# Kernel tuning notes

Measured on AMD Instinct MI355X. Metric: run time of the kernel, lower is better.

## Reference

```python
import jax, jax.numpy as jnp
import numpy as np

N_EMBD = 1024
N_HEAD = 16
HEAD_DIM = N_EMBD // N_HEAD
B, S = 4, 1024


def setup_inputs() -> dict:
    key = jax.random.key(0)
    k1, k2, k3 = jax.random.split(key, 3)
    scale = 0.02
    return {
        "x": jax.random.normal(k1, (B, S, N_EMBD), dtype=jnp.float32),
        "Wqkv": jax.random.normal(k2, (N_EMBD, 3 * N_EMBD), dtype=jnp.float32) * scale,
        "bqkv": jnp.zeros((3 * N_EMBD,), dtype=jnp.float32),
        "Wproj": jax.random.normal(k3, (N_EMBD, N_EMBD), dtype=jnp.float32) * scale,
        "bproj": jnp.zeros((N_EMBD,), dtype=jnp.float32),
    }


def reference(x, Wqkv, bqkv, Wproj, bproj):
    b, s, e = x.shape
    qkv = x @ Wqkv + bqkv  # (b, s, 3e)
    q, k, v = jnp.split(qkv, 3, axis=-1)
    # (b, h, s, d)
    q = q.reshape(b, s, N_HEAD, HEAD_DIM).transpose(0, 2, 1, 3)
    k = k.reshape(b, s, N_HEAD, HEAD_DIM).transpose(0, 2, 1, 3)
    v = v.reshape(b, s, N_HEAD, HEAD_DIM).transpose(0, 2, 1, 3)
    scores = jnp.einsum("bhqd,bhkd->bhqk", q, k) / jnp.sqrt(
        jnp.asarray(HEAD_DIM, dtype=x.dtype)
    )
    causal = jnp.tril(jnp.ones((s, s), dtype=bool))  # (s, s)
    scores = jnp.where(causal[None, None, :, :], scores, jnp.asarray(-jnp.inf, dtype=scores.dtype))
    attn = jax.nn.softmax(scores, axis=-1)
    out = jnp.einsum("bhqk,bhkd->bhqd", attn, v)
    out = out.transpose(0, 2, 1, 3).reshape(b, s, e)
    return out @ Wproj + bproj
```

## Files before the change

### kernel.cpp

```cpp
#include <hip/hip_runtime.h>

#define S_LEN 1024
#define EMB   1024
#define NH    16
#define HD    64
#define BATCH 4
#define M_TOT 4096
#define QSZ   (BATCH * NH * S_LEN * HD)

typedef __attribute__((ext_vector_type(4))) float  f32x4;
typedef __attribute__((ext_vector_type(8))) __bf16 bf16x8;

__device__ __forceinline__ unsigned short f2bf(float f) {
  union { float f; unsigned u; } a; a.f = f;
  unsigned r = a.u + 0x7fffu + ((a.u >> 16) & 1u);
  return (unsigned short)(r >> 16);
}

__device__ __forceinline__ float fexp2(float x) {
#if __has_builtin(__builtin_amdgcn_exp2f)
  return __builtin_amdgcn_exp2f(x);
#else
  return exp2f(x);
#endif
}

__global__ __launch_bounds__(256) void prep(
    const float* __restrict__ x, const float* __restrict__ Wqkv,
    const float* __restrict__ Wproj,
    unsigned short* __restrict__ xb, unsigned short* __restrict__ WqkvT,
    unsigned short* __restrict__ WprojT)
{
  __shared__ unsigned short tile[32][33];
  const int bid = blockIdx.x;
  if (bid < 4096) {
    const int i = bid * 256 + threadIdx.x;
    float4 v = ((const float4*)x)[i];
    ushort4 o;
    o.x = f2bf(v.x); o.y = f2bf(v.y); o.z = f2bf(v.z); o.w = f2bf(v.w);
    ((ushort4*)xb)[i] = o;
    return;
  }
  const float* in; unsigned short* out; int N, n0, k0;
  if (bid < 7168) {
    const int b2 = bid - 4096;
    in = Wqkv; out = WqkvT; N = 3 * EMB;
    n0 = (b2 % 96) * 32; k0 = (b2 / 96) * 32;
  } else {
    const int b3 = bid - 7168;
    in = Wproj; out = WprojT; N = EMB;
    n0 = (b3 % 32) * 32; k0 = (b3 / 32) * 32;
  }
  const int tx = threadIdx.x & 31, ty = threadIdx.x >> 5;
  #pragma unroll
  for (int r = ty; r < 32; r += 8)
    tile[r][tx] = f2bf(in[(size_t)(k0 + r) * N + n0 + tx]);
  __syncthreads();
  #pragma unroll
  for (int r = ty; r < 32; r += 8)
    out[(size_t)(n0 + r) * EMB + k0 + tx] = tile[tx][r];
}

template<int EPI>
__global__ __launch_bounds__(512, 4) void gemm_tile(
    const unsigned short* __restrict__ A,
    const unsigned short* __restrict__ Bt,
    const float* __restrict__ bias,
    void* __restrict__ outp,
    int K, int Nout)
{
  __shared__ alignas(16) char smem[65536];
  const int m0 = blockIdx.x * 128, n0 = blockIdx.y * 128;
  const int t = threadIdx.x;
  const int wid = t >> 6, lane = t & 63;
  const int wm = wid >> 2, wn = wid & 3;
  const int lr = lane & 15, lg = lane >> 4;
  const int nkt = K >> 6;

  f32x4 acc[4][2] = {};

  auto STAGE = [&](int b, int kt) {
    const int k0 = kt << 6;
    #pragma unroll
    for (int l = 0; l < 2; ++l) {
      const int L = l * 8192 + t * 16;
      const int row = L >> 7, c = (L >> 4) & 7;
      const int ce = (c ^ (row & 7)) << 3;
      const unsigned short* gA = A  + (size_t)(m0 + row) * K + k0 + ce;
      const unsigned short* gB = Bt + (size_t)(n0 + row) * K + k0 + ce;
      __builtin_amdgcn_global_load_lds(
          (const __attribute__((address_space(1))) unsigned int*)gA,
          (__attribute__((address_space(3))) unsigned int*)(smem + b * 32768 + L),
          16, 0, 0);
      __builtin_amdgcn_global_load_lds(
          (const __attribute__((address_space(1))) unsigned int*)gB,
          (__attribute__((address_space(3))) unsigned int*)(smem + b * 32768 + 16384 + L),
          16, 0, 0);
    }
  };

  STAGE(0, 0);

  for (int kt = 0; kt < nkt; ++kt) {
    const int cur = kt & 1;
    if (kt + 1 < nkt) {
      STAGE(cur ^ 1, kt + 1);
      asm volatile("s_waitcnt vmcnt(4)" ::: "memory");
    } else {
      asm volatile("s_waitcnt vmcnt(0)" ::: "memory");
    }
    __builtin_amdgcn_s_barrier();
    asm volatile("" ::: "memory");

    const char* Ab = smem + cur * 32768;
    const char* Bb = Ab + 16384;
    bf16x8 af[4][2], bfr[2][2];
    #pragma unroll
    for (int i = 0; i < 4; ++i)
      #pragma unroll
      for (int kk = 0; kk < 2; ++kk) {
        const int row = wm * 64 + i * 16 + lr;
        af[i][kk] = *(const bf16x8*)(Ab + row * 128 + (((kk * 4 + lg) ^ (row & 7)) << 4));
      }
    #pragma unroll
    for (int j = 0; j < 2; ++j)
      #pragma unroll
      for (int kk = 0; kk < 2; ++kk) {
        const int row = wn * 32 + j * 16 + lr;
        bfr[j][kk] = *(const bf16x8*)(Bb + row * 128 + (((kk * 4 + lg) ^ (row & 7)) << 4));
      }
    __builtin_amdgcn_s_setprio(1);
    #pragma unroll
    for (int i = 0; i < 4; ++i)
      #pragma unroll
      for (int j = 0; j < 2; ++j)
        #pragma unroll
        for (int kk = 0; kk < 2; ++kk)
          acc[i][j] = __builtin_amdgcn_mfma_f32_16x16x32_bf16(af[i][kk], bfr[j][kk], acc[i][j], 0, 0, 0);
    __builtin_amdgcn_s_setprio(0);

    asm volatile("s_waitcnt lgkmcnt(0)" ::: "memory");
    __builtin_amdgcn_s_barrier();
  }

  if (EPI == 0) {
    unsigned short* O = (unsigned short*)outp;
    const int sec = n0 >> 10;
    if (sec < 2) {
      #pragma unroll
      for (int i = 0; i < 4; ++i)
        #pragma unroll
        for (int j = 0; j < 2; ++j) {
          const int col = n0 + wn * 32 + j * 16 + lr;
          const float bv = bias[col];
          const int cc = col & 1023, h = cc >> 6, d = cc & 63;
          #pragma unroll
          for (int r = 0; r < 4; ++r) {
            const int row = m0 + wm * 64 + i * 16 + lg * 4 + r;
            float v = acc[i][j][r] + bv;
            if (sec == 0) v *= 0.18033688f;
            const int bb = row >> 10, ss = row & 1023;
            O[(size_t)sec * QSZ + (((size_t)(bb * NH + h) * S_LEN + ss) * HD + d)] = f2bf(v);
          }
        }
    } else {
      unsigned short* T = (unsigned short*)smem;
      #pragma unroll
      for (int i = 0; i < 4; ++i)
        #pragma unroll
        for (int j = 0; j < 2; ++j) {
          const int ci = wn * 32 + j * 16 + lr;
          const float bv = bias[n0 + ci];
          union { ushort4 s4; __bf16 b[4]; } pk;
          #pragma unroll
          for (int r = 0; r < 4; ++r) pk.b[r] = (__bf16)(acc[i][j][r] + bv);
          *(ushort4*)(T + ci * 136 + wm * 64 + i * 16 + lg * 4) = pk.s4;
        }
      __syncthreads();
      const int ci = t >> 2, part = t & 3;
      const int cc = (n0 - 2048) + ci;
      const int h = cc >> 6, d = cc & 63;
      const int bb2 = m0 >> 10, sbase = m0 & 1023;
      unsigned short* dst = O + 2ull * QSZ +
          ((size_t)(bb2 * NH + h) * HD + d) * S_LEN + sbase;
      #pragma unroll
      for (int u = 0; u < 4; ++u) {
        const int spos = part * 32 + u * 8;
        *(bf16x8*)(dst + spos) = *(const bf16x8*)(T + ci * 136 + spos);
      }
    }
  } else {
    float* Of = (float*)outp;
    #pragma unroll
    for (int i = 0; i < 4; ++i)
      #pragma unroll
      for (int j = 0; j < 2; ++j) {
        const int col = n0 + wn * 32 + j * 16 + lr;
        const float bv = bias[col];
        #pragma unroll
        for (int r = 0; r < 4; ++r) {
          const int row = m0 + wm * 64 + i * 16 + lg * 4 + r;
          Of[(size_t)row * (size_t)Nout + col] = acc[i][j][r] + bv;
        }
      }
  }
}

__device__ __forceinline__ void group_tile(
    const bf16x8 (&kf)[8], const bf16x8 (&vf)[8], const bf16x8 (&qf)[2],
    int kt, int q0, bool diag, int lr, int lg,
    float& m, float& lp, f32x4 (&o)[4])
{
  f32x4 sacc[4] = {};
  __builtin_amdgcn_s_setprio(1);
  #pragma unroll
  for (int nt = 0; nt < 4; ++nt)
    #pragma unroll
    for (int kk = 0; kk < 2; ++kk)
      sacc[nt] = __builtin_amdgcn_mfma_f32_16x16x32_bf16(kf[nt * 2 + kk], qf[kk], sacc[nt], 0, 0, 0);
  __builtin_amdgcn_s_setprio(0);

  float p[16];
  if (diag) {
    const int q = q0 + lr;
    #pragma unroll
    for (int nt = 0; nt < 4; ++nt)
      #pragma unroll
      for (int r = 0; r < 4; ++r) {
        int k = kt * 64 + nt * 16 + lg * 4 + r;
        p[nt * 4 + r] = (k > q) ? -1e30f : sacc[nt][r];
      }
  } else {
    #pragma unroll
    for (int nt = 0; nt < 4; ++nt)
      #pragma unroll
      for (int r = 0; r < 4; ++r)
        p[nt * 4 + r] = sacc[nt][r];
  }

  float r8[8], r4[4];
  #pragma unroll
  for (int i = 0; i < 8; ++i) r8[i] = fmaxf(p[i], p[i + 8]);
  #pragma unroll
  for (int i = 0; i < 4; ++i) r4[i] = fmaxf(r8[i], r8[i + 4]);
  float pm = fmaxf(fmaxf(r4[0], r4[1]), fmaxf(r4[2], r4[3]));
  if (__any(pm > m + 11.5f)) {
    float px = fmaxf(pm, __shfl_xor(pm, 16, 64));
    px = fmaxf(px, __shfl_xor(px, 32, 64));
    float mn = fmaxf(m, px);
    float fs = fexp2(m - mn);
    lp *= fs;
    #pragma unroll
    for (int dt = 0; dt < 4; ++dt)
      #pragma unroll
      for (int r = 0; r < 4; ++r) o[dt][r] *= fs;
    m = mn;
  }
  #pragma unroll
  for (int i = 0; i < 16; ++i) p[i] = fexp2(p[i] - m);

  float s8[8], s4[4];
  #pragma unroll
  for (int i = 0; i < 8; ++i) s8[i] = p[i] + p[i + 8];
  #pragma unroll
  for (int i = 0; i < 4; ++i) s4[i] = s8[i] + s8[i + 4];
  lp += (s4[0] + s4[1]) + (s4[2] + s4[3]);

  union { unsigned u[8]; __bf16 b[16]; } W;
  #pragma unroll
  for (int i = 0; i < 16; ++i) W.b[i] = (__bf16)p[i];

  const int dl0 = ((2 * (lg & 1) + (lg >> 1)) * 16 + lr) << 2;
  const int dl1 = ((2 * ((lg & 1) ^ 1) + (lg >> 1)) * 16 + lr) << 2;
  const bool oddlg = (lg & 1) != 0;
  const bool hb    = (lg >> 1) != 0;
  union { unsigned u[4]; bf16x8 v; } T0, T1;
  #pragma unroll
  for (int kk = 0; kk < 2; ++kk) {
    #pragma unroll
    for (int c = 0; c < 2; ++c) {
      unsigned vlo = W.u[4 * kk + c];
      unsigned vhi = W.u[4 * kk + 2 + c];
      unsigned s0 = oddlg ? vhi : vlo;
      unsigned s1 = oddlg ? vlo : vhi;
      unsigned r0 = (unsigned)__builtin_amdgcn_ds_permute(dl0, (int)s0);
      unsigned r1 = (unsigned)__builtin_amdgcn_ds_permute(dl1, (int)s1);
      unsigned* T = kk ? T1.u : T0.u;
      T[c]     = hb ? r1 : r0;
      T[2 + c] = hb ? r0 : r1;
    }
  }

  __builtin_amdgcn_s_setprio(1);
  #pragma unroll
  for (int dt = 0; dt < 4; ++dt) {
    o[dt] = __builtin_amdgcn_mfma_f32_16x16x32_bf16(vf[dt * 2 + 0], T0.v, o[dt], 0, 0, 0);
    o[dt] = __builtin_amdgcn_mfma_f32_16x16x32_bf16(vf[dt * 2 + 1], T1.v, o[dt], 0, 0, 0);
  }
  __builtin_amdgcn_s_setprio(0);
}

__device__ __forceinline__ void group_epilogue(
    const f32x4 (&o)[4], float lp, int q0, int lr, int lg,
    char* Ep, unsigned short* __restrict__ attout, int bb, int h)
{
  float l2 = lp + __shfl_xor(lp, 16, 64);
  float l4 = l2 + __shfl_xor(l2, 32, 64);
  float rl = 1.0f / l4;
  #pragma unroll
  for (int dt = 0; dt < 4; ++dt) {
    union { ushort4 s4; __bf16 b[4]; } ov;
    #pragma unroll
    for (int r = 0; r < 4; ++r) ov.b[r] = (__bf16)(o[dt][r] * rl);
    int byt = (lr * 128 + (dt * 16 + lg * 4) * 2) ^ ((lr & 7) << 4);
    *(ushort4*)(Ep + byt) = ov.s4;
  }
  asm volatile("s_waitcnt lgkmcnt(0)" ::: "memory");
  const int lane = lr + lg * 16;
  const int ql = lane >> 2, c = lane & 3;
  #pragma unroll
  for (int s = 0; s < 2; ++s) {
    int byt = (ql * 128 + (c * 16 + s * 8) * 2) ^ ((ql & 7) << 4);
    bf16x8 vrow = *(const bf16x8*)(Ep + byt);
    *(bf16x8*)(attout + (size_t)(bb * S_LEN + q0 + ql) * EMB + h * HD + c * 16 + s * 8) = vrow;
  }
}

__global__ __launch_bounds__(256, 2) void attn_fwd(
    const unsigned short* __restrict__ Q,
    const unsigned short* __restrict__ K,
    const unsigned short* __restrict__ Vt,
    unsigned short* __restrict__ attout)
{
  __shared__ alignas(16) char stage[3][16384];
  __shared__ alignas(16) char Ep_lds[4][2048];
  const int bid = blockIdx.x;
  const int bh   = ((bid & 7) << 3) | ((bid >> 3) & 7);
  const int base = bid >> 6;
  const int wv = threadIdx.x >> 6, lane = threadIdx.x & 63;
  const int pi = base * 4 + wv;
  const int lr = lane & 15, lg = lane >> 4;
  const int nkt  = 16 - base;
  const int nktl = base + 1;
  const int q0h = (63 - pi) * 16, q0l = pi * 16;
  const unsigned short* Qb = Q  + (size_t)bh * (S_LEN * HD);
  const unsigned short* Kh = K  + (size_t)bh * (S_LEN * HD);
  const unsigned short* Vh = Vt + (size_t)bh * (HD * S_LEN);
  const int bb = bh >> 4, h = bh & 15;

  auto STAGE = [&](int b, int kt) {
    char* lb = &stage[b][0];
    #pragma unroll
    for (int j = 0; j < 4; ++j) {
      if (wv < 2) {
        int L = wv * 4096 + j * 1024 + lane * 16;
        int row = L >> 7, c = (L >> 4) & 7;
        const unsigned short* src = Kh + (size_t)(kt * 64 + row) * HD + ((c ^ (row & 7)) << 3);
        __builtin_amdgcn_global_load_lds(
            (const __attribute__((address_space(1))) unsigned int*)src,
            (__attribute__((address_space(3))) unsigned int*)(lb + wv * 4096 + j * 1024),
            16, 0, 0);
      } else {
        int L = (wv - 2) * 4096 + j * 1024 + lane * 16;
        int row = L >> 7, c = (L >> 4) & 7;
        const unsigned short* src = Vh + (size_t)row * S_LEN + kt * 64 + ((c ^ (row & 7)) << 3);
        __builtin_amdgcn_global_load_lds(
            (const __attribute__((address_space(1))) unsigned int*)src,
            (__attribute__((address_space(3))) unsigned int*)(lb + 8192 + (wv - 2) * 4096 + j * 1024),
            16, 0, 0);
      }
    }
  };

  bf16x8 qfh[2], qfl[2];
  #pragma unroll
  for (int kk = 0; kk < 2; ++kk) {
    qfh[kk] = *(const bf16x8*)(Qb + (size_t)(q0h + lr) * HD + kk * 32 + lg * 8);
    qfl[kk] = *(const bf16x8*)(Qb + (size_t)(q0l + lr) * HD + kk * 32 + lg * 8);
  }

  float mh = -1e30f, lph = 0.f, ml = -1e30f, lpl = 0.f;
  f32x4 oh[4] = {}, ol[4] = {};

  STAGE(0, 0);
  STAGE(1, 1);

  for (int kt = 0; kt < nkt; ++kt) {
    if (kt + 2 < nkt) {
      STAGE((kt + 2) % 3, kt + 2);
      asm volatile("s_waitcnt vmcnt(8)" ::: "memory");
    } else if (kt + 1 < nkt) {
      asm volatile("s_waitcnt vmcnt(4)" ::: "memory");
    } else {
      asm volatile("s_waitcnt vmcnt(0)" ::: "memory");
    }
    __builtin_amdgcn_s_barrier();
    asm volatile("" ::: "memory");

    const char* sb = &stage[kt % 3][0];
    bf16x8 kf[8], vf[8];
    #pragma unroll
    for (int nt = 0; nt < 4; ++nt)
      #pragma unroll
      for (int kk = 0; kk < 2; ++kk) {
        const int byt = (nt * 16 + lr) * 128 + ((((kk << 2) + lg) ^ (lr & 7)) << 4);
        kf[nt * 2 + kk] = *(const bf16x8*)(sb + byt);
        vf[nt * 2 + kk] = *(const bf16x8*)(sb + 8192 + byt);
      }

    group_tile(kf, vf, qfh, kt, q0h, kt == nkt - 1, lr, lg, mh, lph, oh);
    if (kt < nktl)
      group_tile(kf, vf, qfl, kt, q0l, kt == nktl - 1, lr, lg, ml, lpl, ol);

    asm volatile("s_waitcnt lgkmcnt(0)" ::: "memory");
    __builtin_amdgcn_s_barrier();
  }

  char* Ep = &Ep_lds[wv][0];
  group_epilogue(oh, lph, q0h, lr, lg, Ep, attout, bb, h);
  group_epilogue(ol, lpl, q0l, lr, lg, Ep, attout, bb, h);
}

extern "C" void kernel_launch(void* const* d_in, const int* in_sizes, int n_in,
                              void* d_out, int out_size, void* d_ws, size_t ws_size,
                              hipStream_t stream) {
  const float* x     = (const float*)d_in[0];
  const float* Wqkv  = (const float*)d_in[1];
  const float* bqkv  = (const float*)d_in[2];
  const float* Wproj = (const float*)d_in[3];
  const float* bproj = (const float*)d_in[4];

  unsigned short* xb     = (unsigned short*)d_ws;
  unsigned short* WqkvT  = xb     + (size_t)M_TOT * EMB;
  unsigned short* WprojT = WqkvT  + (size_t)3 * EMB * EMB;
  unsigned short* qkv    = WprojT + (size_t)EMB * EMB;
  unsigned short* att    = qkv    + 3ull * QSZ;

  prep<<<dim3(8192), dim3(256), 0, stream>>>(x, Wqkv, Wproj, xb, WqkvT, WprojT);

  gemm_tile<0><<<dim3(M_TOT / 128, 3 * EMB / 128), dim3(512), 0, stream>>>(
      xb, WqkvT, bqkv, (void*)qkv, EMB, 0);

  attn_fwd<<<dim3(8 * BATCH * NH), dim3(256), 0, stream>>>(
      qkv, qkv + QSZ, qkv + 2ull * QSZ, att);

  gemm_tile<1><<<dim3(M_TOT / 128, EMB / 128), dim3(512), 0, stream>>>(
      att, WprojT, bproj, d_out, EMB, EMB);
}
```

Baseline: 85.65 us.

## Deepen software pipelines in GEMM and attention, drop trailing barriers

The GEMM mainloop moves from a 64-wide K tile with double buffering to a 32-wide K tile with triple buffering. Each prefetch is issued after the current tile's LDS reads, and the end-of-iteration barrier is removed. The attention kernel goes from three to four K/V stages in the same style, prefetching three tiles ahead with one barrier per iteration. This aims to hide more global latency and cut synchronisation, at the cost of more LDS in attention and half as much MFMA work per barrier in the GEMM.

```diff
diff --git a/kernel.cpp b/kernel.cpp
--- a/kernel.cpp
+++ b/kernel.cpp
@@ -69,78 +69,70 @@
     void* __restrict__ outp,
     int K, int Nout)
 {
-  __shared__ alignas(16) char smem[65536];
+  __shared__ alignas(16) char smem[49152];
   const int m0 = blockIdx.x * 128, n0 = blockIdx.y * 128;
   const int t = threadIdx.x;
   const int wid = t >> 6, lane = t & 63;
   const int wm = wid >> 2, wn = wid & 3;
   const int lr = lane & 15, lg = lane >> 4;
-  const int nkt = K >> 6;
+  const int nkt = K >> 5;
 
   f32x4 acc[4][2] = {};
 
   auto STAGE = [&](int b, int kt) {
-    const int k0 = kt << 6;
-    #pragma unroll
-    for (int l = 0; l < 2; ++l) {
-      const int L = l * 8192 + t * 16;
-      const int row = L >> 7, c = (L >> 4) & 7;
-      const int ce = (c ^ (row & 7)) << 3;
-      const unsigned short* gA = A  + (size_t)(m0 + row) * K + k0 + ce;
-      const unsigned short* gB = Bt + (size_t)(n0 + row) * K + k0 + ce;
-      __builtin_amdgcn_global_load_lds(
-          (const __attribute__((address_space(1))) unsigned int*)gA,
-          (__attribute__((address_space(3))) unsigned int*)(smem + b * 32768 + L),
-          16, 0, 0);
-      __builtin_amdgcn_global_load_lds(
-          (const __attribute__((address_space(1))) unsigned int*)gB,
-          (__attribute__((address_space(3))) unsigned int*)(smem + b * 32768 + 16384 + L),
-          16, 0, 0);
-    }
+    const int k0 = kt << 5;
+    const int L = t * 16;
+    const int row = L >> 6;
+    const int c = (L >> 4) & 3;
+    const int ce = (c ^ (row & 3)) << 3;
+    const unsigned short* gA = A  + (size_t)(m0 + row) * K + k0 + ce;
+    const unsigned short* gB = Bt + (size_t)(n0 + row) * K + k0 + ce;
+    __builtin_amdgcn_global_load_lds(
+        (const __attribute__((address_space(1))) unsigned int*)gA,
+        (__attribute__((address_space(3))) unsigned int*)(smem + b * 16384 + L),
+        16, 0, 0);
+    __builtin_amdgcn_global_load_lds(
+        (const __attribute__((address_space(1))) unsigned int*)gB,
+        (__attribute__((address_space(3))) unsigned int*)(smem + b * 16384 + 8192 + L),
+        16, 0, 0);
   };
 
   STAGE(0, 0);
+  STAGE(1, 1);
 
   for (int kt = 0; kt < nkt; ++kt) {
-    const int cur = kt & 1;
     if (kt + 1 < nkt) {
-      STAGE(cur ^ 1, kt + 1);
-      asm volatile("s_waitcnt vmcnt(4)" ::: "memory");
+      asm volatile("s_waitcnt vmcnt(2)" ::: "memory");
     } else {
       asm volatile("s_waitcnt vmcnt(0)" ::: "memory");
     }
     __builtin_amdgcn_s_barrier();
     asm volatile("" ::: "memory");
 
-    const char* Ab = smem + cur * 32768;
-    const char* Bb = Ab + 16384;
-    bf16x8 af[4][2], bfr[2][2];
+    const char* Ab = smem + (kt % 3) * 16384;
+    const char* Bb = Ab + 8192;
+    bf16x8 af[4], bfr[2];
+    #pragma unroll
+    for (int i = 0; i < 4; ++i) {
+      const int row = wm * 64 + i * 16 + lr;
+      af[i] = *(const bf16x8*)(Ab + row * 64 + ((lg ^ (row & 3)) << 4));
+    }
+    #pragma unroll
+    for (int j = 0; j < 2; ++j) {
+      const int row = wn * 32 + j * 16 + lr;
+      bfr[j] = *(const bf16x8*)(Bb + row * 64 + ((lg ^ (row & 3)) << 4));
+    }
+    if (kt + 2 < nkt) STAGE((kt + 2) % 3, kt + 2);
+
+    __builtin_amdgcn_s_setprio(1);
     #pragma unroll
     for (int i = 0; i < 4; ++i)
       #pragma unroll
-      for (int kk = 0; kk < 2; ++kk) {
-        const int row = wm * 64 + i * 16 + lr;
-        af[i][kk] = *(const bf16x8*)(Ab + row * 128 + (((kk * 4 + lg) ^ (row & 7)) << 4));
-      }
-    #pragma unroll
-    for (int j = 0; j < 2; ++j)
-      #pragma unroll
-      for (int kk = 0; kk < 2; ++kk) {
-        const int row = wn * 32 + j * 16 + lr;
-        bfr[j][kk] = *(const bf16x8*)(Bb + row * 128 + (((kk * 4 + lg) ^ (row & 7)) << 4));
-      }
-    __builtin_amdgcn_s_setprio(1);
-    #pragma unroll
-    for (int i = 0; i < 4; ++i)
-      #pragma unroll
       for (int j = 0; j < 2; ++j)
-        #pragma unroll
-        for (int kk = 0; kk < 2; ++kk)
-          acc[i][j] = __builtin_amdgcn_mfma_f32_16x16x32_bf16(af[i][kk], bfr[j][kk], acc[i][j], 0, 0, 0);
+        acc[i][j] = __builtin_amdgcn_mfma_f32_16x16x32_bf16(af[i], bfr[j], acc[i][j], 0, 0, 0);
     __builtin_amdgcn_s_setprio(0);
 
     asm volatile("s_waitcnt lgkmcnt(0)" ::: "memory");
-    __builtin_amdgcn_s_barrier();
   }
 
   if (EPI == 0) {
@@ -165,6 +157,7 @@
         }
     } else {
       unsigned short* T = (unsigned short*)smem;
+      __syncthreads();
       #pragma unroll
       for (int i = 0; i < 4; ++i)
         #pragma unroll
@@ -332,7 +325,7 @@
     const unsigned short* __restrict__ Vt,
     unsigned short* __restrict__ attout)
 {
-  __shared__ alignas(16) char stage[3][16384];
+  __shared__ alignas(16) char stage[4][16384];
   __shared__ alignas(16) char Ep_lds[4][2048];
   const int bid = blockIdx.x;
   const int bh   = ((bid & 7) << 3) | ((bid >> 3) & 7);
@@ -384,10 +377,10 @@
 
   STAGE(0, 0);
   STAGE(1, 1);
+  STAGE(2, 2);
 
   for (int kt = 0; kt < nkt; ++kt) {
     if (kt + 2 < nkt) {
-      STAGE((kt + 2) % 3, kt + 2);
       asm volatile("s_waitcnt vmcnt(8)" ::: "memory");
     } else if (kt + 1 < nkt) {
       asm volatile("s_waitcnt vmcnt(4)" ::: "memory");
@@ -397,7 +390,7 @@
     __builtin_amdgcn_s_barrier();
     asm volatile("" ::: "memory");
 
-    const char* sb = &stage[kt % 3][0];
+    const char* sb = &stage[kt & 3][0];
     bf16x8 kf[8], vf[8];
     #pragma unroll
     for (int nt = 0; nt < 4; ++nt)
@@ -407,13 +400,13 @@
         kf[nt * 2 + kk] = *(const bf16x8*)(sb + byt);
         vf[nt * 2 + kk] = *(const bf16x8*)(sb + 8192 + byt);
       }
+    if (kt + 3 < nkt) STAGE((kt + 3) & 3, kt + 3);
 
     group_tile(kf, vf, qfh, kt, q0h, kt == nkt - 1, lr, lg, mh, lph, oh);
     if (kt < nktl)
       group_tile(kf, vf, qfl, kt, q0l, kt == nktl - 1, lr, lg, ml, lpl, ol);
 
     asm volatile("s_waitcnt lgkmcnt(0)" ::: "memory");
-    __builtin_amdgcn_s_barrier();
   }
 
   char* Ep = &Ep_lds[wv][0];
```

Measured after the change: 87.95 us. +2.7%, slower.
